# Optimization experiments

Hardware: AMD Instinct MI355X
Metric: run time of the kernel (lower is better)

The kernel has to match this reference:

```python
import jax, jax.numpy as jnp
import numpy as np

B, L, F = 512, 128, 300          # batch, cycles per sample, curve length
D_MODEL = 512
D_LLM = 4096
E = 8                            # num_experts
G = 2                            # num_general_experts
TOP_K = 2
P = TOP_K / E                    # top-p threshold = topK / num_experts
EPS = 1e-9


def setup_inputs() -> dict:
    key = jax.random.key(0)
    ks = jax.random.split(key, 8)
    s_in = 1.0 / np.sqrt(3 * F).astype(np.float32)   # torch Linear init bound
    s_g = 1.0 / np.sqrt(D_LLM).astype(np.float32)
    return {
        "cycle_curve_data": jax.random.normal(ks[0], (B, L, 3, F), jnp.float32),
        "DKP_embeddings": jax.random.normal(ks[1], (B, D_LLM), jnp.float32),
        "W_exp": jax.random.uniform(ks[2], (E, 3 * F, D_MODEL), jnp.float32, -s_in, s_in),
        "b_exp": jax.random.uniform(ks[3], (E, D_MODEL), jnp.float32, -s_in, s_in),
        "W_gen": jax.random.uniform(ks[4], (G, 3 * F, D_MODEL), jnp.float32, -s_in, s_in),
        "b_gen": jax.random.uniform(ks[5], (G, D_MODEL), jnp.float32, -s_in, s_in),
        "W_gate": jax.random.uniform(ks[6], (D_LLM, E), jnp.float32, -s_g, s_g),
        "b_gate": jax.random.uniform(ks[7], (E,), jnp.float32, -s_g, s_g),
    }


def top_p_mask(logits, p):
    # softmax -> sort desc -> cumsum < p (first always kept) -> scatter back
    probs = jax.nn.softmax(logits, axis=-1)
    order = jnp.argsort(-probs, axis=-1)
    cum = jnp.cumsum(jnp.take_along_axis(probs, order, axis=-1), axis=-1)
    m = (cum < p).at[:, 0].set(True)
    rows = jnp.arange(logits.shape[0])[:, None]
    return jnp.zeros(logits.shape, bool).at[rows, order].set(m)


def reference(cycle_curve_data, DKP_embeddings, W_exp, b_exp, W_gen, b_gen, W_gate, b_gate):
    Bsz, Ls = cycle_curve_data.shape[:2]
    x = cycle_curve_data.reshape(Bsz, Ls, -1)            # [B, L, 3F]  (Flatten(start_dim=2))

    # gate (eval path: no noisy gating)
    logits = DKP_embeddings @ W_gate + b_gate            # [B, E]
    mask = top_p_mask(logits, P)
    w = jax.nn.softmax(logits, axis=1) * mask            # masked gate probs
    w = w / (jnp.sum(w, axis=1, keepdims=True) + EPS)    # renormalize (zeros stay zero)

    # dense equivalent of per-expert gather -> Linear -> weighted scatter-combine:
    # tokens with w[b,e]==0 contribute nothing, matching the sparse dispatcher.
    expert_outs = jnp.einsum('blf,efd->ebld', x, W_exp) + b_exp[:, None, None, :]  # [E,B,L,D]
    combined = jnp.einsum('be,ebld->bld', w, expert_outs).astype(jnp.bfloat16)     # [B,L,D] bf16

    # general experts run over the full batch and accumulate (bf16 + f32 -> f32)
    gen = jnp.einsum('blf,gfd->bld', x, W_gen) + jnp.sum(b_gen, axis=0)            # [B,L,D]
    return combined + gen
```

## Files before the change

kernel.cpp:

```cpp
#include <hip/hip_runtime.h>
#include <stdint.h>

#define NB   512
#define NL   128
#define NK   900
#define NKP  928
#define NKT  29
#define ND   512
#define NDLLM 4096
#define NE   8

typedef __bf16 bf16x8 __attribute__((ext_vector_type(8)));
typedef float  f32x4  __attribute__((ext_vector_type(4)));

__device__ __forceinline__ unsigned short f2bf(float f) {
  union { float f; uint32_t u; } v; v.f = f;
  uint32_t u = v.u;
  return (unsigned short)((u + 0x7fffu + ((u >> 16) & 1u)) >> 16);
}

__global__ __launch_bounds__(256) void gate_kernel(
    const float* __restrict__ dkp,
    const float* __restrict__ Wg,
    const float* __restrict__ bg,
    int* __restrict__ eidx)
{
  const int b = blockIdx.x;
  const int t = threadIdx.x;
  float acc[8];
#pragma unroll
  for (int e = 0; e < 8; ++e) acc[e] = 0.f;
  const float* drow = dkp + (size_t)b * NDLLM;
  for (int k = t; k < NDLLM; k += 256) {
    float d = drow[k];
    const float4* w4 = (const float4*)(Wg + (size_t)k * 8);
    float4 w0 = w4[0], w1 = w4[1];
    acc[0] += d * w0.x; acc[1] += d * w0.y; acc[2] += d * w0.z; acc[3] += d * w0.w;
    acc[4] += d * w1.x; acc[5] += d * w1.y; acc[6] += d * w1.z; acc[7] += d * w1.w;
  }
#pragma unroll
  for (int e = 0; e < 8; ++e)
    for (int off = 32; off >= 1; off >>= 1)
      acc[e] += __shfl_down(acc[e], off, 64);

  __shared__ float red[4][8];
  const int wave = t >> 6, lane = t & 63;
  if (lane == 0) {
#pragma unroll
    for (int e = 0; e < 8; ++e) red[wave][e] = acc[e];
  }
  __syncthreads();
  if (t == 0) {
    float best = -1e30f; int bi = 0;
#pragma unroll
    for (int e = 0; e < 8; ++e) {
      float v = red[0][e] + red[1][e] + red[2][e] + red[3][e] + bg[e];
      if (v > best) { best = v; bi = e; }
    }
    eidx[b] = bi;
  }
}

__global__ __launch_bounds__(256) void pack_kernel(
    const float* __restrict__ Wexp,
    const float* __restrict__ Wgen,
    unsigned short* __restrict__ Wt)
{
  const int nt = blockIdx.x;
  const int kt = blockIdx.y;
  const int e  = blockIdx.z;
  const int k0 = kt * 32, n0 = nt * 64;
  __shared__ float tile[32][65];
  const int t = threadIdx.x;
#pragma unroll
  for (int i = 0; i < 8; ++i) {
    int idx = t + i * 256;
    int k = idx >> 6, n = idx & 63;
    int kg = k0 + k;
    float v = 0.f;
    if (kg < NK) {
      size_t off = (size_t)kg * ND + n0 + n;
      v = Wexp[(size_t)e * NK * ND + off] + Wgen[off] + Wgen[(size_t)NK * ND + off];
    }
    tile[k][n] = v;
  }
  __syncthreads();
#pragma unroll
  for (int i = 0; i < 8; ++i) {
    int idx = t + i * 256;
    int n = idx >> 5, k = idx & 31;
    Wt[((size_t)e * ND + n0 + n) * NKP + k0 + k] = f2bf(tile[k][n]);
  }
}

__global__ __launch_bounds__(256) void bias_kernel(
    const float* __restrict__ bexp, const float* __restrict__ bgen,
    float* __restrict__ btot)
{
  int i = blockIdx.x * 256 + threadIdx.x;
  int d = i & (ND - 1);
  btot[i] = bexp[i] + bgen[d] + bgen[ND + d];
}

__global__ __launch_bounds__(256) void gemm_kernel(
    const float* __restrict__ x,
    const unsigned short* __restrict__ Wt,
    const float* __restrict__ btot,
    const int* __restrict__ eidx,
    float* __restrict__ out)
{
  __shared__ unsigned short As[NL * 32];
  __shared__ unsigned short Bs[128 * 32];

  const int b  = blockIdx.y;
  const int nt = blockIdx.x;
  const int t  = threadIdx.x;
  const int lane = t & 63;
  const int w  = t >> 6;
  const int wm = (w >> 1) * 64;
  const int wn = (w & 1) * 64;
  const int ln = lane & 15;
  const int kq = lane >> 4;

  const int e = eidx[b];
  const float* xb = x + (size_t)b * NL * NK;
  const unsigned short* wtb = Wt + ((size_t)e * ND + (size_t)nt * 128) * NKP;

  f32x4 acc[4][4];
  const f32x4 zero = {0.f, 0.f, 0.f, 0.f};
#pragma unroll
  for (int i = 0; i < 4; ++i)
#pragma unroll
    for (int j = 0; j < 4; ++j) acc[i][j] = zero;

  const int al  = t >> 3;
  const int akc = t & 7;

  for (int kt = 0; kt < NKT; ++kt) {
    const int k0 = kt * 32;
    __syncthreads();

#pragma unroll
    for (int p = 0; p < 2; ++p) {
      int c = t + p * 256;
      int n = c >> 2, kc8 = c & 3;
      const unsigned short* src = wtb + (size_t)n * NKP + k0 + kc8 * 8;
      unsigned short* dst = &Bs[c * 8];
      __builtin_amdgcn_global_load_lds(
          (__attribute__((address_space(1))) void*)(void*)src,
          (__attribute__((address_space(3))) void*)dst, 16, 0, 0);
    }

#pragma unroll
    for (int p = 0; p < 4; ++p) {
      int l  = al + p * 32;
      int kg = k0 + akc * 4;
      ushort4 h;
      if (kg < NK) {
        const float4 v = *(const float4*)(xb + (size_t)l * NK + kg);
        h.x = f2bf(v.x); h.y = f2bf(v.y); h.z = f2bf(v.z); h.w = f2bf(v.w);
      } else {
        h.x = 0; h.y = 0; h.z = 0; h.w = 0;
      }
      *(ushort4*)&As[l * 32 + akc * 4] = h;
    }
    __syncthreads();

    bf16x8 af[4], bv[4];
#pragma unroll
    for (int mi = 0; mi < 4; ++mi)
      af[mi] = *(bf16x8*)&As[(wm + mi * 16 + ln) * 32 + kq * 8];
#pragma unroll
    for (int ni = 0; ni < 4; ++ni)
      bv[ni] = *(bf16x8*)&Bs[(wn + ni * 16 + ln) * 32 + kq * 8];
#pragma unroll
    for (int mi = 0; mi < 4; ++mi)
#pragma unroll
      for (int ni = 0; ni < 4; ++ni)
        acc[mi][ni] = __builtin_amdgcn_mfma_f32_16x16x32_bf16(
            af[mi], bv[ni], acc[mi][ni], 0, 0, 0);
  }

  const float* bt = btot + (size_t)e * ND;
  const int nb = nt * 128;
#pragma unroll
  for (int ni = 0; ni < 4; ++ni) {
    int ncol = nb + wn + ni * 16 + ln;
    float bias = bt[ncol];
#pragma unroll
    for (int mi = 0; mi < 4; ++mi) {
      int l0 = wm + mi * 16 + kq * 4;
      float* op = out + ((size_t)b * NL + l0) * ND + ncol;
#pragma unroll
      for (int r = 0; r < 4; ++r)
        op[(size_t)r * ND] = acc[mi][ni][r] + bias;
    }
  }
}

extern "C" void kernel_launch(void* const* d_in, const int* in_sizes, int n_in,
                              void* d_out, int out_size, void* d_ws, size_t ws_size,
                              hipStream_t stream) {
  const float* x     = (const float*)d_in[0];
  const float* dkp   = (const float*)d_in[1];
  const float* Wexp  = (const float*)d_in[2];
  const float* bexp  = (const float*)d_in[3];
  const float* Wgen  = (const float*)d_in[4];
  const float* bgen  = (const float*)d_in[5];
  const float* Wgate = (const float*)d_in[6];
  const float* bgate = (const float*)d_in[7];
  float* out = (float*)d_out;

  int*   eidx = (int*)d_ws;
  float* btot = (float*)((char*)d_ws + 2048);
  unsigned short* Wt = (unsigned short*)((char*)d_ws + 18432);

  gate_kernel<<<NB, 256, 0, stream>>>(dkp, Wgate, bgate, eidx);
  pack_kernel<<<dim3(8, NKT, NE), 256, 0, stream>>>(Wexp, Wgen, Wt);
  bias_kernel<<<16, 256, 0, stream>>>(bexp, bgen, btot);
  gemm_kernel<<<dim3(4, NB), 256, 0, stream>>>(x, Wt, btot, eidx, out);
}
```

Baseline: 594.5 us.

## Load GEMM operands directly into registers, drop LDS staging, remap blocks per XCD

The GEMM no longer stages A and B tiles through shared memory with barriers. Each lane loads its MFMA fragments straight from global memory, converting x from fp32 to bf16 in registers, and the K tail is handled as a separate peeled step. The grid is flattened and remapped so each XCD handles a contiguous range of batches, which aims to improve L2 reuse of the expert weights, and launch bounds now request three blocks per SIMD. This removes the barrier and LDS traffic, but each lane now issues strided, less coalesced global loads, and A rows are reloaded by two waves.

```diff
diff --git a/kernel.cpp b/kernel.cpp
--- a/kernel.cpp
+++ b/kernel.cpp
@@ -5,7 +5,6 @@
 #define NL   128
 #define NK   900
 #define NKP  928
-#define NKT  29
 #define ND   512
 #define NDLLM 4096
 #define NE   8
@@ -102,77 +101,86 @@
   btot[i] = bexp[i] + bgen[d] + bgen[ND + d];
 }
 
-__global__ __launch_bounds__(256) void gemm_kernel(
+__global__ __launch_bounds__(256, 3) void gemm_kernel(
     const float* __restrict__ x,
     const unsigned short* __restrict__ Wt,
     const float* __restrict__ btot,
     const int* __restrict__ eidx,
     float* __restrict__ out)
 {
-  __shared__ unsigned short As[NL * 32];
-  __shared__ unsigned short Bs[128 * 32];
-
-  const int b  = blockIdx.y;
-  const int nt = blockIdx.x;
-  const int t  = threadIdx.x;
+  const int g   = blockIdx.x;
+  const int xcd = g & 7;
+  const int j   = g >> 3;
+  const int nt  = j & 3;
+  const int b   = xcd * 64 + (j >> 2);
+
+  const int t    = threadIdx.x;
   const int lane = t & 63;
-  const int w  = t >> 6;
-  const int wm = (w >> 1) * 64;
-  const int wn = (w & 1) * 64;
-  const int ln = lane & 15;
-  const int kq = lane >> 4;
+  const int w    = t >> 6;
+  const int wm   = (w >> 1) * 64;
+  const int wn   = (w & 1) * 64;
+  const int ln   = lane & 15;
+  const int kq   = lane >> 4;
 
   const int e = eidx[b];
   const float* xb = x + (size_t)b * NL * NK;
   const unsigned short* wtb = Wt + ((size_t)e * ND + (size_t)nt * 128) * NKP;
 
+  const float* arow[4];
+  const unsigned short* brow[4];
+#pragma unroll
+  for (int mi = 0; mi < 4; ++mi)
+    arow[mi] = xb + (size_t)(wm + mi * 16 + ln) * NK;
+#pragma unroll
+  for (int ni = 0; ni < 4; ++ni)
+    brow[ni] = wtb + (size_t)(wn + ni * 16 + ln) * NKP;
+
   f32x4 acc[4][4];
   const f32x4 zero = {0.f, 0.f, 0.f, 0.f};
 #pragma unroll
   for (int i = 0; i < 4; ++i)
 #pragma unroll
-    for (int j = 0; j < 4; ++j) acc[i][j] = zero;
-
-  const int al  = t >> 3;
-  const int akc = t & 7;
-
-  for (int kt = 0; kt < NKT; ++kt) {
-    const int k0 = kt * 32;
-    __syncthreads();
-
-#pragma unroll
-    for (int p = 0; p < 2; ++p) {
-      int c = t + p * 256;
-      int n = c >> 2, kc8 = c & 3;
-      const unsigned short* src = wtb + (size_t)n * NKP + k0 + kc8 * 8;
-      unsigned short* dst = &Bs[c * 8];
-      __builtin_amdgcn_global_load_lds(
-          (__attribute__((address_space(1))) void*)(void*)src,
-          (__attribute__((address_space(3))) void*)dst, 16, 0, 0);
-    }
-
-#pragma unroll
-    for (int p = 0; p < 4; ++p) {
-      int l  = al + p * 32;
-      int kg = k0 + akc * 4;
-      ushort4 h;
-      if (kg < NK) {
-        const float4 v = *(const float4*)(xb + (size_t)l * NK + kg);
-        h.x = f2bf(v.x); h.y = f2bf(v.y); h.z = f2bf(v.z); h.w = f2bf(v.w);
-      } else {
-        h.x = 0; h.y = 0; h.z = 0; h.w = 0;
+    for (int jj = 0; jj < 4; ++jj) acc[i][jj] = zero;
+
+#pragma unroll 2
+  for (int kt = 0; kt < 28; ++kt) {
+    const int kk = kt * 32 + kq * 8;
+    bf16x8 bv[4], af[4];
+#pragma unroll
+    for (int ni = 0; ni < 4; ++ni)
+      bv[ni] = *(const bf16x8*)(brow[ni] + kk);
+#pragma unroll
+    for (int mi = 0; mi < 4; ++mi) {
+      const float4 v0 = *(const float4*)(arow[mi] + kk);
+      const float4 v1 = *(const float4*)(arow[mi] + kk + 4);
+      bf16x8 a;
+      a[0] = (__bf16)v0.x; a[1] = (__bf16)v0.y; a[2] = (__bf16)v0.z; a[3] = (__bf16)v0.w;
+      a[4] = (__bf16)v1.x; a[5] = (__bf16)v1.y; a[6] = (__bf16)v1.z; a[7] = (__bf16)v1.w;
+      af[mi] = a;
+    }
+#pragma unroll
+    for (int mi = 0; mi < 4; ++mi)
+#pragma unroll
+      for (int ni = 0; ni < 4; ++ni)
+        acc[mi][ni] = __builtin_amdgcn_mfma_f32_16x16x32_bf16(
+            af[mi], bv[ni], acc[mi][ni], 0, 0, 0);
+  }
+
+  {
+    const int kk = 896 + kq * 8;
+    bf16x8 bv[4], af[4];
+#pragma unroll
+    for (int ni = 0; ni < 4; ++ni)
+      bv[ni] = *(const bf16x8*)(brow[ni] + kk);
+#pragma unroll
+    for (int mi = 0; mi < 4; ++mi) {
+      bf16x8 a = {0, 0, 0, 0, 0, 0, 0, 0};
+      if (kq == 0) {
+        const float4 v0 = *(const float4*)(arow[mi] + 896);
+        a[0] = (__bf16)v0.x; a[1] = (__bf16)v0.y; a[2] = (__bf16)v0.z; a[3] = (__bf16)v0.w;
       }
-      *(ushort4*)&As[l * 32 + akc * 4] = h;
-    }
-    __syncthreads();
-
-    bf16x8 af[4], bv[4];
-#pragma unroll
-    for (int mi = 0; mi < 4; ++mi)
-      af[mi] = *(bf16x8*)&As[(wm + mi * 16 + ln) * 32 + kq * 8];
-#pragma unroll
-    for (int ni = 0; ni < 4; ++ni)
-      bv[ni] = *(bf16x8*)&Bs[(wn + ni * 16 + ln) * 32 + kq * 8];
+      af[mi] = a;
+    }
 #pragma unroll
     for (int mi = 0; mi < 4; ++mi)
 #pragma unroll
@@ -216,7 +224,7 @@
   unsigned short* Wt = (unsigned short*)((char*)d_ws + 18432);
 
   gate_kernel<<<NB, 256, 0, stream>>>(dkp, Wgate, bgate, eidx);
-  pack_kernel<<<dim3(8, NKT, NE), 256, 0, stream>>>(Wexp, Wgen, Wt);
+  pack_kernel<<<dim3(8, 29, NE), 256, 0, stream>>>(Wexp, Wgen, Wt);
   bias_kernel<<<16, 256, 0, stream>>>(bexp, bgen, btot);
-  gemm_kernel<<<dim3(4, NB), 256, 0, stream>>>(x, Wt, btot, eidx, out);
-}
+  gemm_kernel<<<2048, 256, 0, stream>>>(x, Wt, btot, eidx, out);
+}
```

Result: slower. 667.7 us (+12.3%).
